# Optimization experiments

Hardware: AMD Instinct MI355X
Metric: run time of the kernel (lower is better)

Reference implementation:

```python
import jax, jax.numpy as jnp
import numpy as np

B, D, N, K = 8, 3, 65536, 64
EPS = 1e-8

def setup_inputs() -> dict:
    key = jax.random.key(0)
    k1, k2, k3 = jax.random.split(key, 3)
    return {
        "template_features": jax.random.normal(k1, (B, D, N), dtype=jnp.float32),
        "source_features": jax.random.normal(k2, (B, D, N), dtype=jnp.float32),
        "W": jax.random.normal(k3, (D, K), dtype=jnp.float32),
    }

def _gamma(features_t, W):
    # features_t: (B,N,D); logits: (B,K,N); softmax over points (dim=2, as in torch code)
    logits = jnp.einsum('bnd,dk->bkn', features_t, W)
    return jax.nn.softmax(logits, axis=2)

def _gmm_params(gamma, pts):
    # gamma: (B,K,N), pts: (B,N,D)
    n = gamma.shape[2]
    Npi = gamma.sum(axis=2) + EPS                       # (B,K)
    pi = Npi / n
    g = gamma / (Npi[:, :, None] + EPS)                 # (B,K,N)
    mu = jnp.einsum('bkn,bnd->bkd', g, pts)             # weighted mean
    # second moment; exact central form: sum_n g (x-mu)(x-mu)^T = Exx - (2 - s) mu mu^T
    Exx = jnp.einsum('bkn,bnd,bne->bkde', g, pts, pts)
    s = g.sum(axis=2)                                   # (B,K), ~1 (not exactly, due to eps)
    outer = mu[..., :, None] * mu[..., None, :]
    sigma = (Exx - (2.0 - s)[..., None, None] * outer) / (Npi[:, :, None, None] + EPS)
    return pi, mu, sigma

def _estimate_transform(mu_x, pi_x, mu_y, pi_y):
    cx = jnp.sum(mu_x * pi_x[..., None], axis=1, keepdims=True)   # (B,1,D)
    cy = jnp.sum(mu_y * pi_y[..., None], axis=1, keepdims=True)
    mu_x_c = mu_x - cx
    mu_y_c = mu_y - cy
    Wm = jnp.einsum('bkd,bke->bde', pi_x[..., None] * mu_y_c, mu_x_c)  # (B,D,D)
    U, S, Vh = jnp.linalg.svd(Wm, full_matrices=False)
    R = jnp.matmul(U, Vh)
    det = jnp.linalg.det(R)
    Vh = Vh.at[:, :, -1].multiply(jnp.sign(det)[:, None])
    R = jnp.matmul(U, Vh)
    T = cy[:, 0, :] - jnp.einsum('bde,be->bd', R, cx[:, 0, :])
    return R, T

def reference(template_features, source_features, W):
    template_pts = jnp.swapaxes(template_features, 1, 2)   # (B,N,D)
    source_pts = jnp.swapaxes(source_features, 1, 2)
    t_gamma = _gamma(template_pts, W)
    s_gamma = _gamma(source_pts, W)
    t_pi, t_mu, t_sigma = _gmm_params(t_gamma, template_pts)
    s_pi, s_mu, s_sigma = _gmm_params(s_gamma, source_pts)
    R, T = _estimate_transform(s_mu, s_pi, t_mu, t_pi)
    aligned = jnp.matmul(source_pts, jnp.swapaxes(R, 1, 2)) + T[:, None, :]
    return aligned
```

## Files before the change

### kernel.cpp

```cpp
#include <hip/hip_runtime.h>

#define N_PTS 65536
#define BATCH 8
#define KCL   64
#define CHUNK 1024
#define LOG2E 1.44269504088896340736f

typedef float f32x2 __attribute__((ext_vector_type(2)));
typedef float f32x4 __attribute__((ext_vector_type(4)));

__device__ __forceinline__ double drcp(double x) {
    double r = (double)(1.0f / (float)x);
    r = r * (2.0 - x * r);
    r = r * (2.0 - x * r);
    return r;
}

__device__ __forceinline__ float hw_exp2(float x) {
    return __builtin_amdgcn_exp2f(x);
}

__global__ __launch_bounds__(256) void k_sum(const float* __restrict__ tmpl,
                                             const float* __restrict__ srcf,
                                             const float* __restrict__ Wmat,
                                             float* __restrict__ Zs,
                                             float* __restrict__ Ss) {
    const int bx    = blockIdx.x;
    const int set   = bx >> 9;
    const int b     = (bx >> 6) & 7;
    const int chunk = bx & 63;
    const float* feat = set ? srcf : tmpl;
    const int n0 = chunk * CHUNK;

    __shared__ float xs[3][CHUNK];
    __shared__ float red[4][KCL][8];

    const int tid  = threadIdx.x;
    const int lane = tid & 63;
    const int wv   = tid >> 6;

    const float* base = feat + (size_t)b * 3 * N_PTS + n0;
#pragma unroll
    for (int j = 0; j < 3; ++j) {
        const float* g = base + (size_t)j * N_PTS + wv * 256 + lane * 4;
        __builtin_amdgcn_global_load_lds(
            (const __attribute__((address_space(1))) void*)g,
            (__attribute__((address_space(3))) void*)&xs[j][wv * 256],
            16, 0, 0);
    }
    __syncthreads();

    const int h  = lane >> 5;
    const int cA = lane & 31;
    const float w0a = Wmat[cA] * LOG2E,        w0b = Wmat[cA + 32] * LOG2E;
    const float w1a = Wmat[KCL + cA] * LOG2E,  w1b = Wmat[KCL + cA + 32] * LOG2E;
    const float w2a = Wmat[2*KCL + cA] * LOG2E, w2b = Wmat[2*KCL + cA + 32] * LOG2E;
    const f32x2 w0av = {w0a, w0a}, w1av = {w1a, w1a}, w2av = {w2a, w2a};
    const f32x2 w0bv = {w0b, w0b}, w1bv = {w1b, w1b}, w2bv = {w2b, w2b};

    f32x2 zA = {0,0}, s0A = {0,0}, s1A = {0,0}, s2A = {0,0};
    f32x2 zB = {0,0}, s0B = {0,0}, s1B = {0,0}, s2B = {0,0};

    const f32x4* lp0 = (const f32x4*)&xs[0][0];
    const f32x4* lp1 = (const f32x4*)&xs[1][0];
    const f32x4* lp2 = (const f32x4*)&xs[2][0];

#pragma unroll 2
    for (int it = 0; it < 32; ++it) {
        const int q = wv * 64 + it * 2 + h;
        f32x4 a = lp0[q];
        f32x4 c = lp1[q];
        f32x4 d = lp2[q];
#pragma unroll
        for (int p = 0; p < 2; ++p) {
            f32x2 ax = p ? a.zw : a.xy;
            f32x2 cx = p ? c.zw : c.xy;
            f32x2 dx = p ? d.zw : d.xy;
            {
                f32x2 l = __builtin_elementwise_fma(ax, w0av,
                            __builtin_elementwise_fma(cx, w1av, dx * w2av));
                f32x2 e = {hw_exp2(l.x), hw_exp2(l.y)};
                zA += e;
                s0A = __builtin_elementwise_fma(e, ax, s0A);
                s1A = __builtin_elementwise_fma(e, cx, s1A);
                s2A = __builtin_elementwise_fma(e, dx, s2A);
            }
            {
                f32x2 l = __builtin_elementwise_fma(ax, w0bv,
                            __builtin_elementwise_fma(cx, w1bv, dx * w2bv));
                f32x2 e = {hw_exp2(l.x), hw_exp2(l.y)};
                zB += e;
                s0B = __builtin_elementwise_fma(e, ax, s0B);
                s1B = __builtin_elementwise_fma(e, cx, s1B);
                s2B = __builtin_elementwise_fma(e, dx, s2B);
            }
        }
    }

    red[wv][lane][0] = zA.x + zA.y;
    red[wv][lane][1] = s0A.x + s0A.y;
    red[wv][lane][2] = s1A.x + s1A.y;
    red[wv][lane][3] = s2A.x + s2A.y;
    red[wv][lane][4] = zB.x + zB.y;
    red[wv][lane][5] = s0B.x + s0B.y;
    red[wv][lane][6] = s1B.x + s1B.y;
    red[wv][lane][7] = s2B.x + s2B.y;
    __syncthreads();

    if (tid < KCL) {
        const int cl = tid & 31;
        const int sb = (tid >> 5) * 4;
        float rz = 0, rs0 = 0, rs1 = 0, rs2 = 0;
#pragma unroll
        for (int w = 0; w < 4; ++w) {
            rz  += red[w][cl][sb + 0] + red[w][cl + 32][sb + 0];
            rs0 += red[w][cl][sb + 1] + red[w][cl + 32][sb + 1];
            rs1 += red[w][cl][sb + 2] + red[w][cl + 32][sb + 2];
            rs2 += red[w][cl][sb + 3] + red[w][cl + 32][sb + 3];
        }
        int idx = (set * BATCH + b) * KCL + tid;
        atomicAdd(&Zs[idx], rz);
        atomicAdd(&Ss[idx * 3 + 0], rs0);
        atomicAdd(&Ss[idx * 3 + 1], rs1);
        atomicAdd(&Ss[idx * 3 + 2], rs2);
    }
}

__global__ __launch_bounds__(256) void k_apply(const float* __restrict__ srcf,
                                               const float* __restrict__ Zs,
                                               const float* __restrict__ Ss,
                                               float* __restrict__ out) {
    __shared__ float rt_s[BATCH][12];

    if (threadIdx.x < 64) {
        const int lane = threadIdx.x;
        const int b    = lane >> 3;
        const int sub  = lane & 7;

        const double inv_npi = 1.0 / (1.0 + 2e-8);
        const double pi_c = (1.0 + 1e-8) / (double)N_PTS;

        double Mt[3] = {0, 0, 0}, Ms[3] = {0, 0, 0};
        double P[3][3] = {{0,0,0},{0,0,0},{0,0,0}};
        for (int kk = 0; kk < 8; ++kk) {
            int k  = sub * 8 + kk;
            int it = b * KCL + k;
            int is = (BATCH + b) * KCL + k;
            double izt = inv_npi * drcp((double)Zs[it]);
            double izs = inv_npi * drcp((double)Zs[is]);
            double mt[3], ms[3];
            for (int d = 0; d < 3; ++d) {
                mt[d] = (double)Ss[it * 3 + d] * izt;
                ms[d] = (double)Ss[is * 3 + d] * izs;
                Mt[d] += mt[d];
                Ms[d] += ms[d];
            }
            for (int d = 0; d < 3; ++d)
                for (int e = 0; e < 3; ++e)
                    P[d][e] += mt[d] * ms[e];
        }
        for (int m = 1; m <= 4; m <<= 1) {
            for (int d = 0; d < 3; ++d) {
                Mt[d] += __shfl_xor(Mt[d], m, 64);
                Ms[d] += __shfl_xor(Ms[d], m, 64);
            }
            for (int d = 0; d < 3; ++d)
                for (int e = 0; e < 3; ++e)
                    P[d][e] += __shfl_xor(P[d][e], m, 64);
        }

        double cy[3], cx[3];
        for (int d = 0; d < 3; ++d) { cy[d] = pi_c * Mt[d]; cx[d] = pi_c * Ms[d]; }

        const double coef = 2.0 * pi_c - 64.0 * pi_c * pi_c;
        double A[3][3];
        for (int d = 0; d < 3; ++d)
            for (int e = 0; e < 3; ++e)
                A[d][e] = pi_c * (P[d][e] - coef * Mt[d] * Ms[e]);

        double G[3][3];
        for (int i = 0; i < 3; ++i)
            for (int j = 0; j < 3; ++j) {
                double acc = 0;
                for (int d = 0; d < 3; ++d) acc += A[d][i] * A[d][j];
                G[i][j] = acc;
            }

        double V[3][3] = {{1,0,0},{0,1,0},{0,0,1}};
        const int pairs[3][2] = {{0,1},{0,2},{1,2}};
        const double scale0 = fabs(G[0][0]) + fabs(G[1][1]) + fabs(G[2][2]) + 1e-300;
        for (int sweep = 0; sweep < 10; ++sweep) {
            double off = fabs(G[0][1]) + fabs(G[0][2]) + fabs(G[1][2]);
            if (off < 1e-28 * scale0) break;
            for (int pi_i = 0; pi_i < 3; ++pi_i) {
                int p = pairs[pi_i][0], q = pairs[pi_i][1];
                double apq = G[p][q];
                if (fabs(apq) < 1e-30 * scale0) continue;
                double tau = (G[q][q] - G[p][p]) * drcp(2.0 * apq);
                double t = ((tau >= 0) ? 1.0 : -1.0) * drcp(fabs(tau) + sqrt(1.0 + tau * tau));
                double c = drcp(sqrt(1.0 + t * t));
                double s = t * c;
                double gpp = G[p][p], gqq = G[q][q];
                G[p][p] = gpp - t * apq;
                G[q][q] = gqq + t * apq;
                G[p][q] = G[q][p] = 0.0;
                int r = 3 - p - q;
                double grp = G[r][p], grq = G[r][q];
                G[r][p] = G[p][r] = c * grp - s * grq;
                G[r][q] = G[q][r] = s * grp + c * grq;
                for (int rr = 0; rr < 3; ++rr) {
                    double vrp = V[rr][p], vrq = V[rr][q];
                    V[rr][p] = c * vrp - s * vrq;
                    V[rr][q] = s * vrp + c * vrq;
                }
            }
        }

        double invs[3];
        for (int i = 0; i < 3; ++i) {
            double lam = G[i][i];
            invs[i] = drcp(sqrt(lam > 1e-300 ? lam : 1e-300));
        }
        double M[3][3];
        for (int i = 0; i < 3; ++i)
            for (int j = 0; j < 3; ++j) {
                double acc = 0;
                for (int m2 = 0; m2 < 3; ++m2) acc += V[i][m2] * V[j][m2] * invs[m2];
                M[i][j] = acc;
            }
        double R0[3][3];
        for (int d = 0; d < 3; ++d)
            for (int e = 0; e < 3; ++e) {
                double acc = 0;
                for (int m2 = 0; m2 < 3; ++m2) acc += A[d][m2] * M[m2][e];
                R0[d][e] = acc;
            }

        double det = R0[0][0] * (R0[1][1] * R0[2][2] - R0[1][2] * R0[2][1])
                   - R0[0][1] * (R0[1][0] * R0[2][2] - R0[1][2] * R0[2][0])
                   + R0[0][2] * (R0[1][0] * R0[2][1] - R0[1][1] * R0[2][0]);
        double sg = (det >= 0.0) ? 1.0 : -1.0;
        R0[0][2] *= sg; R0[1][2] *= sg; R0[2][2] *= sg;

        double T[3];
        for (int d = 0; d < 3; ++d)
            T[d] = cy[d] - (R0[d][0] * cx[0] + R0[d][1] * cx[1] + R0[d][2] * cx[2]);

        if (sub == 0) {
            rt_s[b][0] = (float)R0[0][0]; rt_s[b][1] = (float)R0[0][1]; rt_s[b][2] = (float)R0[0][2];
            rt_s[b][3] = (float)R0[1][0]; rt_s[b][4] = (float)R0[1][1]; rt_s[b][5] = (float)R0[1][2];
            rt_s[b][6] = (float)R0[2][0]; rt_s[b][7] = (float)R0[2][1]; rt_s[b][8] = (float)R0[2][2];
            rt_s[b][9] = (float)T[0]; rt_s[b][10] = (float)T[1]; rt_s[b][11] = (float)T[2];
        }
    }
    __syncthreads();

    const int t = blockIdx.x * 256 + threadIdx.x;
#pragma unroll
    for (int i = 0; i < 4; ++i) {
        int idx = t + i * 131072;
        int b = idx >> 16;
        int n = idx & (N_PTS - 1);
        const float* rt = rt_s[b];
        const float* base = srcf + (size_t)b * 3 * N_PTS;
        float x0 = base[n];
        float x1 = base[N_PTS + n];
        float x2 = base[2 * N_PTS + n];
        float y0 = fmaf(rt[0], x0, fmaf(rt[1], x1, fmaf(rt[2], x2, rt[9])));
        float y1 = fmaf(rt[3], x0, fmaf(rt[4], x1, fmaf(rt[5], x2, rt[10])));
        float y2 = fmaf(rt[6], x0, fmaf(rt[7], x1, fmaf(rt[8], x2, rt[11])));
        size_t o = (size_t)idx * 3;
        out[o + 0] = y0;
        out[o + 1] = y1;
        out[o + 2] = y2;
    }
}

extern "C" void kernel_launch(void* const* d_in, const int* in_sizes, int n_in,
                              void* d_out, int out_size, void* d_ws, size_t ws_size,
                              hipStream_t stream) {
    const float* tmpl = (const float*)d_in[0];
    const float* srcf = (const float*)d_in[1];
    const float* Wmat = (const float*)d_in[2];
    float* out = (float*)d_out;

    float* Zs = (float*)d_ws;
    float* Ss = (float*)d_ws + 1024;

    (void)hipMemsetAsync(d_ws, 0, 4096 * sizeof(float), stream);

    k_sum<<<1024, 256, 0, stream>>>(tmpl, srcf, Wmat, Zs, Ss);
    k_apply<<<512, 256, 0, stream>>>(srcf, Zs, Ss, out);
}
```

Before: 92.40 us.

## Replace atomic accumulation with per-block partials and a single-block solve kernel

k_sum now writes per-block partial sums to a workspace buffer instead of issuing global float atomics. A new one-block k_solve kernel reduces those partials and computes R and T once. k_apply then only loads the 96 transform values. This removes the memset, the atomic contention, and the redundant SVD solve that every k_apply block used to run, at the cost of an extra kernel launch and a serial single-block reduction over 1 MB of partials.

```diff
diff --git a/kernel.cpp b/kernel.cpp
--- a/kernel.cpp
+++ b/kernel.cpp
@@ -23,8 +23,7 @@
 __global__ __launch_bounds__(256) void k_sum(const float* __restrict__ tmpl,
                                              const float* __restrict__ srcf,
                                              const float* __restrict__ Wmat,
-                                             float* __restrict__ Zs,
-                                             float* __restrict__ Ss) {
+                                             float* __restrict__ part) {
     const int bx    = blockIdx.x;
     const int set   = bx >> 9;
     const int b     = (bx >> 6) & 7;
@@ -52,8 +51,8 @@
 
     const int h  = lane >> 5;
     const int cA = lane & 31;
-    const float w0a = Wmat[cA] * LOG2E,        w0b = Wmat[cA + 32] * LOG2E;
-    const float w1a = Wmat[KCL + cA] * LOG2E,  w1b = Wmat[KCL + cA + 32] * LOG2E;
+    const float w0a = Wmat[cA] * LOG2E,         w0b = Wmat[cA + 32] * LOG2E;
+    const float w1a = Wmat[KCL + cA] * LOG2E,   w1b = Wmat[KCL + cA + 32] * LOG2E;
     const float w2a = Wmat[2*KCL + cA] * LOG2E, w2b = Wmat[2*KCL + cA + 32] * LOG2E;
     const f32x2 w0av = {w0a, w0a}, w1av = {w1a, w1a}, w2av = {w2a, w2a};
     const f32x2 w0bv = {w0b, w0b}, w1bv = {w1b, w1b}, w2bv = {w2b, w2b};
@@ -118,22 +117,37 @@
             rs1 += red[w][cl][sb + 2] + red[w][cl + 32][sb + 2];
             rs2 += red[w][cl][sb + 3] + red[w][cl + 32][sb + 3];
         }
-        int idx = (set * BATCH + b) * KCL + tid;
-        atomicAdd(&Zs[idx], rz);
-        atomicAdd(&Ss[idx * 3 + 0], rs0);
-        atomicAdd(&Ss[idx * 3 + 1], rs1);
-        atomicAdd(&Ss[idx * 3 + 2], rs2);
-    }
-}
-
-__global__ __launch_bounds__(256) void k_apply(const float* __restrict__ srcf,
-                                               const float* __restrict__ Zs,
-                                               const float* __restrict__ Ss,
-                                               float* __restrict__ out) {
-    __shared__ float rt_s[BATCH][12];
-
-    if (threadIdx.x < 64) {
-        const int lane = threadIdx.x;
+        float4 v = {rz, rs0, rs1, rs2};
+        ((float4*)part)[bx * 64 + tid] = v;
+    }
+}
+
+__global__ __launch_bounds__(256) void k_solve(const float* __restrict__ part,
+                                               float* __restrict__ RT) {
+    __shared__ float Zr[16][64];
+    __shared__ float Sr[16][64][3];
+
+    const int tid = threadIdx.x;
+    const float4* p = (const float4*)part;
+#pragma unroll
+    for (int cc = 0; cc < 4; ++cc) {
+        const int c  = tid + cc * 256;
+        const int sb = c >> 6;
+        const int k  = c & 63;
+        const int base = sb * 4096 + k;
+        float z = 0, s0 = 0, s1 = 0, s2 = 0;
+#pragma unroll 8
+        for (int ch = 0; ch < 64; ++ch) {
+            float4 v = p[base + ch * 64];
+            z += v.x; s0 += v.y; s1 += v.z; s2 += v.w;
+        }
+        Zr[sb][k] = z;
+        Sr[sb][k][0] = s0; Sr[sb][k][1] = s1; Sr[sb][k][2] = s2;
+    }
+    __syncthreads();
+
+    if (tid < 64) {
+        const int lane = tid;
         const int b    = lane >> 3;
         const int sub  = lane & 7;
 
@@ -143,15 +157,13 @@
         double Mt[3] = {0, 0, 0}, Ms[3] = {0, 0, 0};
         double P[3][3] = {{0,0,0},{0,0,0},{0,0,0}};
         for (int kk = 0; kk < 8; ++kk) {
-            int k  = sub * 8 + kk;
-            int it = b * KCL + k;
-            int is = (BATCH + b) * KCL + k;
-            double izt = inv_npi * drcp((double)Zs[it]);
-            double izs = inv_npi * drcp((double)Zs[is]);
+            int k = sub * 8 + kk;
+            double izt = inv_npi * drcp((double)Zr[b][k]);
+            double izs = inv_npi * drcp((double)Zr[8 + b][k]);
             double mt[3], ms[3];
             for (int d = 0; d < 3; ++d) {
-                mt[d] = (double)Ss[it * 3 + d] * izt;
-                ms[d] = (double)Ss[is * 3 + d] * izs;
+                mt[d] = (double)Sr[b][k][d] * izt;
+                ms[d] = (double)Sr[8 + b][k][d] * izs;
                 Mt[d] += mt[d];
                 Ms[d] += ms[d];
             }
@@ -193,24 +205,24 @@
             double off = fabs(G[0][1]) + fabs(G[0][2]) + fabs(G[1][2]);
             if (off < 1e-28 * scale0) break;
             for (int pi_i = 0; pi_i < 3; ++pi_i) {
-                int p = pairs[pi_i][0], q = pairs[pi_i][1];
-                double apq = G[p][q];
+                int p2 = pairs[pi_i][0], q = pairs[pi_i][1];
+                double apq = G[p2][q];
                 if (fabs(apq) < 1e-30 * scale0) continue;
-                double tau = (G[q][q] - G[p][p]) * drcp(2.0 * apq);
+                double tau = (G[q][q] - G[p2][p2]) * drcp(2.0 * apq);
                 double t = ((tau >= 0) ? 1.0 : -1.0) * drcp(fabs(tau) + sqrt(1.0 + tau * tau));
                 double c = drcp(sqrt(1.0 + t * t));
                 double s = t * c;
-                double gpp = G[p][p], gqq = G[q][q];
-                G[p][p] = gpp - t * apq;
+                double gpp = G[p2][p2], gqq = G[q][q];
+                G[p2][p2] = gpp - t * apq;
                 G[q][q] = gqq + t * apq;
-                G[p][q] = G[q][p] = 0.0;
-                int r = 3 - p - q;
-                double grp = G[r][p], grq = G[r][q];
-                G[r][p] = G[p][r] = c * grp - s * grq;
+                G[p2][q] = G[q][p2] = 0.0;
+                int r = 3 - p2 - q;
+                double grp = G[r][p2], grq = G[r][q];
+                G[r][p2] = G[p2][r] = c * grp - s * grq;
                 G[r][q] = G[q][r] = s * grp + c * grq;
                 for (int rr = 0; rr < 3; ++rr) {
-                    double vrp = V[rr][p], vrq = V[rr][q];
-                    V[rr][p] = c * vrp - s * vrq;
+                    double vrp = V[rr][p2], vrq = V[rr][q];
+                    V[rr][p2] = c * vrp - s * vrq;
                     V[rr][q] = s * vrp + c * vrq;
                 }
             }
@@ -247,12 +259,20 @@
             T[d] = cy[d] - (R0[d][0] * cx[0] + R0[d][1] * cx[1] + R0[d][2] * cx[2]);
 
         if (sub == 0) {
-            rt_s[b][0] = (float)R0[0][0]; rt_s[b][1] = (float)R0[0][1]; rt_s[b][2] = (float)R0[0][2];
-            rt_s[b][3] = (float)R0[1][0]; rt_s[b][4] = (float)R0[1][1]; rt_s[b][5] = (float)R0[1][2];
-            rt_s[b][6] = (float)R0[2][0]; rt_s[b][7] = (float)R0[2][1]; rt_s[b][8] = (float)R0[2][2];
-            rt_s[b][9] = (float)T[0]; rt_s[b][10] = (float)T[1]; rt_s[b][11] = (float)T[2];
-        }
-    }
+            float* rt = RT + b * 12;
+            rt[0] = (float)R0[0][0]; rt[1]  = (float)R0[0][1]; rt[2]  = (float)R0[0][2];
+            rt[3] = (float)R0[1][0]; rt[4]  = (float)R0[1][1]; rt[5]  = (float)R0[1][2];
+            rt[6] = (float)R0[2][0]; rt[7]  = (float)R0[2][1]; rt[8]  = (float)R0[2][2];
+            rt[9] = (float)T[0];     rt[10] = (float)T[1];     rt[11] = (float)T[2];
+        }
+    }
+}
+
+__global__ __launch_bounds__(256) void k_apply(const float* __restrict__ srcf,
+                                               const float* __restrict__ RT,
+                                               float* __restrict__ out) {
+    __shared__ float rt_s[96];
+    if (threadIdx.x < 96) rt_s[threadIdx.x] = RT[threadIdx.x];
     __syncthreads();
 
     const int t = blockIdx.x * 256 + threadIdx.x;
@@ -261,7 +281,7 @@
         int idx = t + i * 131072;
         int b = idx >> 16;
         int n = idx & (N_PTS - 1);
-        const float* rt = rt_s[b];
+        const float* rt = &rt_s[b * 12];
         const float* base = srcf + (size_t)b * 3 * N_PTS;
         float x0 = base[n];
         float x1 = base[N_PTS + n];
@@ -284,11 +304,10 @@
     const float* Wmat = (const float*)d_in[2];
     float* out = (float*)d_out;
 
-    float* Zs = (float*)d_ws;
-    float* Ss = (float*)d_ws + 1024;
-
-    (void)hipMemsetAsync(d_ws, 0, 4096 * sizeof(float), stream);
-
-    k_sum<<<1024, 256, 0, stream>>>(tmpl, srcf, Wmat, Zs, Ss);
-    k_apply<<<512, 256, 0, stream>>>(srcf, Zs, Ss, out);
-}
+    float* part = (float*)d_ws;
+    float* RT   = (float*)d_ws + 262144;
+
+    k_sum<<<1024, 256, 0, stream>>>(tmpl, srcf, Wmat, part);
+    k_solve<<<1, 256, 0, stream>>>(part, RT);
+    k_apply<<<512, 256, 0, stream>>>(srcf, RT, out);
+}
```

Measured after the change: 100.1 us. 1.08x slower.
